# Optimization experiments

Hardware: AMD Instinct MI355X
Metric: run time of the kernel (lower is better)

Reference implementation:

```python
import jax, jax.numpy as jnp
import numpy as np

E, S, Q, NN_NODES, R = 2048, 256, 25, 36, 15
H = 128  # MLP hidden width


def setup_inputs() -> dict:
    key = jax.random.key(0)
    ks = jax.random.split(key, 16)
    g = lambda k, shape, scale=1.0: (jax.random.normal(k, shape, dtype=jnp.float32) * scale)
    inp = {
        "nodes": g(ks[0], (E, NN_NODES, 2)),
        "W1": g(ks[1], (2, H), 1.0 / np.sqrt(2.0)),
        "b1": jnp.zeros((H,), jnp.float32),
        "W2": g(ks[2], (H, H), 1.0 / np.sqrt(H)),
        "b2": jnp.zeros((H,), jnp.float32),
        "W3": g(ks[3], (H, H), 1.0 / np.sqrt(H)),
        "b3": jnp.zeros((H,), jnp.float32),
        "W4": g(ks[4], (H, 1), 1.0 / np.sqrt(H)),
        "b4": jnp.zeros((1,), jnp.float32),
        # 2nd-derivative interpolation matrices of the inter basis B at the
        # sub-element quadrature points (shared across big elements).
        "Ixx": g(ks[5], (S, Q, NN_NODES), 0.1),
        "Iyy": g(ks[6], (S, Q, NN_NODES), 0.1),
        # per-big-element 2x2 Hessian change-of-coordinates map (B_DD_inter)
        "B_DD": g(ks[7], (E, 2, 2)),
        "w_quad": jax.random.uniform(ks[8], (Q,), dtype=jnp.float32),
        # test-function values at quadrature points (b.Base)
        "Base": g(ks[9], (Q, R)),
        # per-sub-element Jacobians and precomputed RHS projections F_total
        "J": jax.random.uniform(ks[10], (E, S), dtype=jnp.float32),
        "F": g(ks[11], (E, S, R)),
    }
    return inp


def _mlp(x, W1, b1, W2, b2, W3, b3, W4, b4):
    h = jnp.tanh(x @ W1 + b1)
    h = jnp.tanh(h @ W2 + b2)
    h = jnp.tanh(h @ W3 + b3)
    return h @ W4 + b4


def reference(nodes, W1, b1, W2, b2, W3, b3, W4, b4,
              Ixx, Iyy, B_DD, w_quad, Base, J, F):
    # NN evaluated once per big element at its interpolation nodes: [E, n_nodes]
    ev = _mlp(nodes.reshape(-1, 2), W1, b1, W2, b2, W3, b3, W4, b4)
    ev = ev.reshape(E, NN_NODES)
    d2x = jnp.einsum("sqn,en->esq", Ixx, ev)
    d2y = jnp.einsum("sqn,en->esq", Iyy, ev)
    grad_second = jnp.stack([d2x, d2y], axis=2)           # [E,S,2,Q]
    # B_DD_inter @ grad_second^T, per big element
    grad_second = jnp.einsum("eij,esjq->esiq", B_DD, grad_second)
    integrand_1 = grad_second.sum(axis=2)                 # [E,S,Q]
    # u_NN_el[r] = -J * sum_q w[q] * Base[q,r] * integrand_1[q]
    u_el = -J[:, :, None] * jnp.einsum("q,qr,esq->esr", w_quad, Base, integrand_1)
    res = u_el - F                                        # [E,S,R]
    # loss_element = mean over test functions, summed over all (big, sub) elements
    return jnp.sum(jnp.mean(jnp.square(res), axis=-1))
```

## Files before the change

kernel.cpp:

```cpp
#include <hip/hip_runtime.h>

#define EN 2048
#define SN 256
#define QN 25
#define NNODES 36
#define RN 15
#define HN 128

typedef __attribute__((ext_vector_type(8))) short short8;
typedef __attribute__((ext_vector_type(4))) float f32x4;
typedef __attribute__((ext_vector_type(2))) unsigned int uint2v;

__device__ __forceinline__ unsigned short f2bf(float f) {
    unsigned int u = __float_as_uint(f);
    u += 0x7fffu + ((u >> 16) & 1u);
    return (unsigned short)(u >> 16);
}
__device__ __forceinline__ float bf2f(unsigned short h) {
    return __uint_as_float(((unsigned int)h) << 16);
}
__device__ __forceinline__ float fast_tanh(float x) {
    float xs = x * 2.885390082f;
    xs = fminf(fmaxf(xs, -60.f), 60.f);
    float e = __builtin_amdgcn_exp2f(xs);
    float r = __builtin_amdgcn_rcpf(e + 1.f);
    return fmaf(-2.f, r, 1.f);
}

__device__ __forceinline__ void load_W(const float* __restrict__ W,
                                       unsigned short (*Ws)[136], int t)
{
    const int n = t & 127;
    const int h = t >> 7;
    #pragma unroll
    for (int kk = 0; kk < 16; kk++) {
        const int k0 = (kk * 2 + h) * 4;
        const float a0 = W[(k0 + 0) * HN + n];
        const float a1 = W[(k0 + 1) * HN + n];
        const float a2 = W[(k0 + 2) * HN + n];
        const float a3 = W[(k0 + 3) * HN + n];
        uint2v pk;
        pk[0] = (unsigned)f2bf(a0) | ((unsigned)f2bf(a1) << 16);
        pk[1] = (unsigned)f2bf(a2) | ((unsigned)f2bf(a3) << 16);
        *(uint2v*)&Ws[n][k0] = pk;
    }
}

__device__ __forceinline__ void mfma_layer(unsigned short (*Hs)[136],
                                           const unsigned short (*Ws)[136],
                                           const float* __restrict__ bias,
                                           int wv, int rowA, int quad)
{
    const int r0 = wv * 32;
    short8 afrag[2][4];
    #pragma unroll
    for (int rt = 0; rt < 2; rt++)
        #pragma unroll
        for (int kt = 0; kt < 4; kt++)
            afrag[rt][kt] = *(const short8*)&Hs[r0 + rt * 16 + rowA][kt * 32 + quad * 8];

    f32x4 acc[2][8];
    const f32x4 zero = {0.f, 0.f, 0.f, 0.f};
    #pragma unroll
    for (int rt = 0; rt < 2; rt++)
        #pragma unroll
        for (int nt = 0; nt < 8; nt++) acc[rt][nt] = zero;

    #pragma unroll
    for (int nt = 0; nt < 8; nt++) {
        #pragma unroll
        for (int kt = 0; kt < 4; kt++) {
            const short8 bfrag = *(const short8*)&Ws[nt * 16 + rowA][kt * 32 + quad * 8];
            acc[0][nt] = __builtin_amdgcn_mfma_f32_16x16x32_bf16(afrag[0][kt], bfrag, acc[0][nt], 0, 0, 0);
            acc[1][nt] = __builtin_amdgcn_mfma_f32_16x16x32_bf16(afrag[1][kt], bfrag, acc[1][nt], 0, 0, 0);
        }
    }
    #pragma unroll
    for (int nt = 0; nt < 8; nt++) {
        const int col = nt * 16 + rowA;
        const float bv = bias[col];
        #pragma unroll
        for (int rt = 0; rt < 2; rt++) {
            #pragma unroll
            for (int rg = 0; rg < 4; rg++) {
                const float v = fast_tanh(acc[rt][nt][rg] + bv);
                Hs[r0 + rt * 16 + quad * 4 + rg][col] = f2bf(v);
            }
        }
    }
}

#define MLP_BLOCKS 576
#define MC_BLOCKS 1080

__global__ __launch_bounds__(256, 2)
void prep_kernel(const float* __restrict__ nodes,
                 const float* __restrict__ W1, const float* __restrict__ b1,
                 const float* __restrict__ W2, const float* __restrict__ b2,
                 const float* __restrict__ W3, const float* __restrict__ b3,
                 const float* __restrict__ W4, const float* __restrict__ b4,
                 const float* __restrict__ B_DD,
                 const float* __restrict__ Ixx, const float* __restrict__ Iyy,
                 const float* __restrict__ wq, const float* __restrict__ Base,
                 float* __restrict__ evc, float* __restrict__ Mc,
                 float* __restrict__ out)
{
    __shared__ unsigned short Hs[128][136];
    __shared__ unsigned short Ws[128][136];
    __shared__ float WB[QN * 16];
    const int bid = blockIdx.x;
    const int t   = threadIdx.x;

    if (bid < MLP_BLOCKS) {
        const int lane = t & 63;
        const int wv   = t >> 6;
        const int rowA = lane & 15;
        const int quad = lane >> 4;

        {
            const int p  = t >> 1;
            const int P  = bid * 128 + p;
            const float x0 = nodes[2 * P], x1 = nodes[2 * P + 1];
            const int n0 = (t & 1) * 64;
            #pragma unroll
            for (int i = 0; i < 16; i++) {
                const int n = n0 + 4 * i;
                const float4 wa = *(const float4*)(W1 + n);
                const float4 wb = *(const float4*)(W1 + HN + n);
                const float4 bb = *(const float4*)(b1 + n);
                const float h0 = fast_tanh(fmaf(x0, wa.x, fmaf(x1, wb.x, bb.x)));
                const float h1 = fast_tanh(fmaf(x0, wa.y, fmaf(x1, wb.y, bb.y)));
                const float h2 = fast_tanh(fmaf(x0, wa.z, fmaf(x1, wb.z, bb.z)));
                const float h3 = fast_tanh(fmaf(x0, wa.w, fmaf(x1, wb.w, bb.w)));
                uint2v pk;
                pk[0] = (unsigned)f2bf(h0) | ((unsigned)f2bf(h1) << 16);
                pk[1] = (unsigned)f2bf(h2) | ((unsigned)f2bf(h3) << 16);
                *(uint2v*)&Hs[p][n] = pk;
            }
        }
        load_W(W2, Ws, t);
        __syncthreads();
        mfma_layer(Hs, Ws, b2, wv, rowA, quad);
        __syncthreads();
        load_W(W3, Ws, t);
        __syncthreads();
        mfma_layer(Hs, Ws, b3, wv, rowA, quad);
        {
            const int p  = t >> 1;
            const int k0 = (t & 1) * 64;
            float d = 0.f;
            #pragma unroll
            for (int i = 0; i < 8; i++) {
                const short8 h = *(const short8*)&Hs[p][k0 + 8 * i];
                const float4 wA = *(const float4*)(W4 + k0 + 8 * i);
                const float4 wB = *(const float4*)(W4 + k0 + 8 * i + 4);
                d = fmaf(bf2f((unsigned short)h[0]), wA.x, d);
                d = fmaf(bf2f((unsigned short)h[1]), wA.y, d);
                d = fmaf(bf2f((unsigned short)h[2]), wA.z, d);
                d = fmaf(bf2f((unsigned short)h[3]), wA.w, d);
                d = fmaf(bf2f((unsigned short)h[4]), wB.x, d);
                d = fmaf(bf2f((unsigned short)h[5]), wB.y, d);
                d = fmaf(bf2f((unsigned short)h[6]), wB.z, d);
                d = fmaf(bf2f((unsigned short)h[7]), wB.w, d);
            }
            d += __shfl_xor(d, 1, 64);
            if ((t & 1) == 0) {
                const float ev = d + b4[0];
                const int P  = bid * 128 + p;
                const int e  = P / NNODES;
                const int ne = P - e * NNODES;
                const float c0 = B_DD[4 * e + 0] + B_DD[4 * e + 2];
                const float c1 = B_DD[4 * e + 1] + B_DD[4 * e + 3];
                evc[e * 72 + ne]      = c0 * ev;
                evc[e * 72 + 36 + ne] = c1 * ev;
            }
        }
    } else {
        if (bid == MLP_BLOCKS && t == 0) out[0] = 0.f;
        for (int i = t; i < QN * 16; i += 256) {
            const int q = i >> 4, r = i & 15;
            if (r < RN) WB[i] = wq[q] * Base[q * RN + r];
        }
        __syncthreads();
        const int o = (bid - MLP_BLOCKS) * 256 + t;
        const int c  = o % 72;
        const int sr = o / 72;
        const int r  = sr % RN;
        const int s  = sr / RN;
        const float* __restrict__ I = (c < NNODES) ? Ixx : Iyy;
        const int n = (c < NNODES) ? c : (c - NNODES);
        float a0 = 0.f, a1 = 0.f;
        #pragma unroll
        for (int q = 0; q < QN - 1; q += 2) {
            a0 = fmaf(WB[q * 16 + r],       I[(s * QN + q) * NNODES + n],     a0);
            a1 = fmaf(WB[(q + 1) * 16 + r], I[(s * QN + q + 1) * NNODES + n], a1);
        }
        a0 = fmaf(WB[(QN - 1) * 16 + r], I[(s * QN + QN - 1) * NNODES + n], a0);
        Mc[o] = a0 + a1;
    }
}

__global__ __launch_bounds__(256, 4)
void loss_kernel(const float* __restrict__ Mc, const float* __restrict__ evcg,
                 const float* __restrict__ J, const float* __restrict__ F,
                 float* __restrict__ out)
{
    const int t  = threadIdx.x;
    const int r  = t & 15;
    const int s  = (blockIdx.x & 15) * 16 + (t >> 4);
    const int e0 = (int)(blockIdx.x >> 4) * 16;
    const int rr = (r < RN) ? r : (RN - 1);
    const float vmask = (r < RN) ? 1.f : 0.f;

    float mc[72];
    {
        const float4* __restrict__ mp = (const float4*)(Mc + ((size_t)s * RN + rr) * 72);
        #pragma unroll
        for (int i = 0; i < 18; i++) {
            const float4 v = mp[i];
            mc[4*i+0] = v.x; mc[4*i+1] = v.y; mc[4*i+2] = v.z; mc[4*i+3] = v.w;
        }
    }

    const float* __restrict__ Jp = J + (size_t)e0 * SN + s;
    const float* __restrict__ Fp = F + ((size_t)e0 * SN + s) * RN + rr;
    const float* __restrict__ ev = evcg + (size_t)e0 * 72;

    float acc = 0.f;
    #pragma unroll 1
    for (int ei = 0; ei < 16; ei++) {
        const float Jv = *Jp;
        const float Fv = *Fp;
        float d0 = 0.f, d1 = 0.f, d2 = 0.f, d3 = 0.f;
        #pragma unroll
        for (int n = 0; n < 72; n += 4) {
            d0 = fmaf(ev[n + 0], mc[n + 0], d0);
            d1 = fmaf(ev[n + 1], mc[n + 1], d1);
            d2 = fmaf(ev[n + 2], mc[n + 2], d2);
            d3 = fmaf(ev[n + 3], mc[n + 3], d3);
        }
        const float d = (d0 + d1) + (d2 + d3);
        float res = fmaf(-Jv, d, -Fv);
        res *= vmask;
        acc = fmaf(res, res, acc);
        Jp += SN;
        Fp += SN * RN;
        ev += 72;
    }
    acc *= (1.f / (float)RN);

    #pragma unroll
    for (int off = 32; off; off >>= 1)
        acc += __shfl_down(acc, off, 64);
    __shared__ float wsum[4];
    const int lane = t & 63, wv = t >> 6;
    if (lane == 0) wsum[wv] = acc;
    __syncthreads();
    if (t == 0) atomicAdd(out, (wsum[0] + wsum[1]) + (wsum[2] + wsum[3]));
}

extern "C" void kernel_launch(void* const* d_in, const int* in_sizes, int n_in,
                              void* d_out, int out_size, void* d_ws, size_t ws_size,
                              hipStream_t stream)
{
    (void)in_sizes; (void)n_in; (void)out_size; (void)ws_size;
    const float* nodes = (const float*)d_in[0];
    const float* W1   = (const float*)d_in[1];
    const float* b1   = (const float*)d_in[2];
    const float* W2   = (const float*)d_in[3];
    const float* b2   = (const float*)d_in[4];
    const float* W3   = (const float*)d_in[5];
    const float* b3   = (const float*)d_in[6];
    const float* W4   = (const float*)d_in[7];
    const float* b4   = (const float*)d_in[8];
    const float* Ixx  = (const float*)d_in[9];
    const float* Iyy  = (const float*)d_in[10];
    const float* B_DD = (const float*)d_in[11];
    const float* wq   = (const float*)d_in[12];
    const float* Base = (const float*)d_in[13];
    const float* J    = (const float*)d_in[14];
    const float* F    = (const float*)d_in[15];
    float* out = (float*)d_out;
    float* evc = (float*)d_ws;
    float* Mc  = (float*)((char*)d_ws + EN * 72 * sizeof(float));

    prep_kernel<<<MLP_BLOCKS + MC_BLOCKS, 256, 0, stream>>>(
        nodes, W1, b1, W2, b2, W3, b3, W4, b4, B_DD, Ixx, Iyy, wq, Base,
        evc, Mc, out);
    loss_kernel<<<2048, 256, 0, stream>>>(Mc, evc, J, F, out);
}
```

Baseline: 172.6 us.

## Compute loss contraction as bf16 MFMA GEMM over padded evc and Mc

Replaces the per-thread scalar FMA dot product in the loss kernel with a GEMM on bf16 MFMA instructions: evc (E x 96) times Mc (S*R x 96). The prep kernel now writes both operands as bf16, zero-padded from K=72 to K=96, and the residual/square reduction is fused into the MFMA epilogue. This moves the dominant contraction from scalar ALUs to matrix cores and halves intermediate storage. In exchange it rounds to bf16, which adds precision error, and J/F are read with strided, uncoalesced accesses in the epilogue.

```diff
diff --git a/kernel.cpp b/kernel.cpp
--- a/kernel.cpp
+++ b/kernel.cpp
@@ -6,6 +6,8 @@
 #define NNODES 36
 #define RN 15
 #define HN 128
+#define KP 96
+#define NTOT (SN * RN)
 
 typedef __attribute__((ext_vector_type(8))) short short8;
 typedef __attribute__((ext_vector_type(4))) float f32x4;
@@ -91,7 +93,7 @@
 }
 
 #define MLP_BLOCKS 576
-#define MC_BLOCKS 1080
+#define MC_BLOCKS 1440
 
 __global__ __launch_bounds__(256, 2)
 void prep_kernel(const float* __restrict__ nodes,
@@ -102,7 +104,8 @@
                  const float* __restrict__ B_DD,
                  const float* __restrict__ Ixx, const float* __restrict__ Iyy,
                  const float* __restrict__ wq, const float* __restrict__ Base,
-                 float* __restrict__ evc, float* __restrict__ Mc,
+                 unsigned short* __restrict__ evcb,
+                 unsigned short* __restrict__ Mcb,
                  float* __restrict__ out)
 {
     __shared__ unsigned short Hs[128][136];
@@ -171,8 +174,10 @@
                 const int ne = P - e * NNODES;
                 const float c0 = B_DD[4 * e + 0] + B_DD[4 * e + 2];
                 const float c1 = B_DD[4 * e + 1] + B_DD[4 * e + 3];
-                evc[e * 72 + ne]      = c0 * ev;
-                evc[e * 72 + 36 + ne] = c1 * ev;
+                evcb[e * KP + ne]          = f2bf(c0 * ev);
+                evcb[e * KP + NNODES + ne] = f2bf(c1 * ev);
+                if (ne < KP - 2 * NNODES)
+                    evcb[e * KP + 2 * NNODES + ne] = 0;
             }
         }
     } else {
@@ -183,78 +188,87 @@
         }
         __syncthreads();
         const int o = (bid - MLP_BLOCKS) * 256 + t;
-        const int c  = o % 72;
-        const int sr = o / 72;
-        const int r  = sr % RN;
-        const int s  = sr / RN;
+        const int c = o % KP;
+        const int n = o / KP;
+        if (c >= 2 * NNODES) { Mcb[o] = 0; return; }
+        const int r = n % RN;
+        const int s = n / RN;
         const float* __restrict__ I = (c < NNODES) ? Ixx : Iyy;
-        const int n = (c < NNODES) ? c : (c - NNODES);
+        const int cn = (c < NNODES) ? c : (c - NNODES);
         float a0 = 0.f, a1 = 0.f;
         #pragma unroll
         for (int q = 0; q < QN - 1; q += 2) {
-            a0 = fmaf(WB[q * 16 + r],       I[(s * QN + q) * NNODES + n],     a0);
-            a1 = fmaf(WB[(q + 1) * 16 + r], I[(s * QN + q + 1) * NNODES + n], a1);
-        }
-        a0 = fmaf(WB[(QN - 1) * 16 + r], I[(s * QN + QN - 1) * NNODES + n], a0);
-        Mc[o] = a0 + a1;
+            a0 = fmaf(WB[q * 16 + r],       I[(s * QN + q) * NNODES + cn],     a0);
+            a1 = fmaf(WB[(q + 1) * 16 + r], I[(s * QN + q + 1) * NNODES + cn], a1);
+        }
+        a0 = fmaf(WB[(QN - 1) * 16 + r], I[(s * QN + QN - 1) * NNODES + cn], a0);
+        Mcb[o] = f2bf(a0 + a1);
     }
 }
 
 __global__ __launch_bounds__(256, 4)
-void loss_kernel(const float* __restrict__ Mc, const float* __restrict__ evcg,
+void loss_kernel(const unsigned short* __restrict__ evcb,
+                 const unsigned short* __restrict__ Mcb,
                  const float* __restrict__ J, const float* __restrict__ F,
                  float* __restrict__ out)
 {
-    const int t  = threadIdx.x;
-    const int r  = t & 15;
-    const int s  = (blockIdx.x & 15) * 16 + (t >> 4);
-    const int e0 = (int)(blockIdx.x >> 4) * 16;
-    const int rr = (r < RN) ? r : (RN - 1);
-    const float vmask = (r < RN) ? 1.f : 0.f;
-
-    float mc[72];
-    {
-        const float4* __restrict__ mp = (const float4*)(Mc + ((size_t)s * RN + rr) * 72);
-        #pragma unroll
-        for (int i = 0; i < 18; i++) {
-            const float4 v = mp[i];
-            mc[4*i+0] = v.x; mc[4*i+1] = v.y; mc[4*i+2] = v.z; mc[4*i+3] = v.w;
-        }
-    }
-
-    const float* __restrict__ Jp = J + (size_t)e0 * SN + s;
-    const float* __restrict__ Fp = F + ((size_t)e0 * SN + s) * RN + rr;
-    const float* __restrict__ ev = evcg + (size_t)e0 * 72;
-
-    float acc = 0.f;
-    #pragma unroll 1
-    for (int ei = 0; ei < 16; ei++) {
-        const float Jv = *Jp;
-        const float Fv = *Fp;
-        float d0 = 0.f, d1 = 0.f, d2 = 0.f, d3 = 0.f;
-        #pragma unroll
-        for (int n = 0; n < 72; n += 4) {
-            d0 = fmaf(ev[n + 0], mc[n + 0], d0);
-            d1 = fmaf(ev[n + 1], mc[n + 1], d1);
-            d2 = fmaf(ev[n + 2], mc[n + 2], d2);
-            d3 = fmaf(ev[n + 3], mc[n + 3], d3);
-        }
-        const float d = (d0 + d1) + (d2 + d3);
-        float res = fmaf(-Jv, d, -Fv);
-        res *= vmask;
-        acc = fmaf(res, res, acc);
-        Jp += SN;
-        Fp += SN * RN;
-        ev += 72;
-    }
-    acc *= (1.f / (float)RN);
+    const int t    = threadIdx.x;
+    const int lane = t & 63;
+    const int wv   = t >> 6;
+    const int rowA = lane & 15;
+    const int quad = lane >> 4;
+    const int m0 = (blockIdx.x & 31) * 64;
+    const int n0 = (blockIdx.x >> 5) * 128 + wv * 32;
+
+    f32x4 acc[4][2];
+    const f32x4 zero = {0.f, 0.f, 0.f, 0.f};
+    #pragma unroll
+    for (int mt = 0; mt < 4; mt++)
+        #pragma unroll
+        for (int nt = 0; nt < 2; nt++) acc[mt][nt] = zero;
+
+    #pragma unroll
+    for (int kt = 0; kt < 3; kt++) {
+        short8 a[4], b[2];
+        #pragma unroll
+        for (int mt = 0; mt < 4; mt++)
+            a[mt] = *(const short8*)&evcb[(m0 + mt * 16 + rowA) * KP + kt * 32 + quad * 8];
+        #pragma unroll
+        for (int nt = 0; nt < 2; nt++)
+            b[nt] = *(const short8*)&Mcb[(n0 + nt * 16 + rowA) * KP + kt * 32 + quad * 8];
+        #pragma unroll
+        for (int mt = 0; mt < 4; mt++)
+            #pragma unroll
+            for (int nt = 0; nt < 2; nt++)
+                acc[mt][nt] = __builtin_amdgcn_mfma_f32_16x16x32_bf16(a[mt], b[nt], acc[mt][nt], 0, 0, 0);
+    }
+
+    float total = 0.f;
+    #pragma unroll
+    for (int nt = 0; nt < 2; nt++) {
+        const int n = n0 + nt * 16 + rowA;
+        const int s = (n * 34953) >> 19;
+        #pragma unroll
+        for (int mt = 0; mt < 4; mt++) {
+            const int eb = m0 + mt * 16 + quad * 4;
+            #pragma unroll
+            for (int rg = 0; rg < 4; rg++) {
+                const int e = eb + rg;
+                const float Jv = J[e * SN + s];
+                const float Fv = F[e * NTOT + n];
+                const float d  = acc[mt][nt][rg];
+                const float res = fmaf(-Jv, d, -Fv);
+                total = fmaf(res, res, total);
+            }
+        }
+    }
+    total *= (1.f / (float)RN);
 
     #pragma unroll
     for (int off = 32; off; off >>= 1)
-        acc += __shfl_down(acc, off, 64);
+        total += __shfl_down(total, off, 64);
     __shared__ float wsum[4];
-    const int lane = t & 63, wv = t >> 6;
-    if (lane == 0) wsum[wv] = acc;
+    if (lane == 0) wsum[wv] = total;
     __syncthreads();
     if (t == 0) atomicAdd(out, (wsum[0] + wsum[1]) + (wsum[2] + wsum[3]));
 }
@@ -281,11 +295,11 @@
     const float* J    = (const float*)d_in[14];
     const float* F    = (const float*)d_in[15];
     float* out = (float*)d_out;
-    float* evc = (float*)d_ws;
-    float* Mc  = (float*)((char*)d_ws + EN * 72 * sizeof(float));
+    unsigned short* evcb = (unsigned short*)d_ws;
+    unsigned short* Mcb  = (unsigned short*)((char*)d_ws + EN * KP * 2);
 
     prep_kernel<<<MLP_BLOCKS + MC_BLOCKS, 256, 0, stream>>>(
         nodes, W1, b1, W2, b2, W3, b3, W4, b4, B_DD, Ixx, Iyy, wq, Base,
-        evc, Mc, out);
-    loss_kernel<<<2048, 256, 0, stream>>>(Mc, evc, J, F, out);
-}
+        evcb, Mcb, out);
+    loss_kernel<<<32 * 30, 256, 0, stream>>>(evcb, Mcb, J, F, out);
+}
```

New measurement: 154.1 us. 1.12x faster.
